# Kernel tuning notes

Hardware: AMD Instinct MI355X
Metric: run time of the kernel (lower is better)

## Reference

```python
import jax, jax.numpy as jnp
import numpy as np

K = 3
EPS = 1e-16

def setup_inputs() -> dict:
    key = jax.random.key(0)
    k1, k2, k3 = jax.random.split(key, 3)
    x = jax.random.normal(k1, (4096, 256), dtype=jnp.float32)
    pos_l = jax.random.normal(k2, (4096, 3), dtype=jnp.float32)
    pos_h = jax.random.normal(k3, (16384, 3), dtype=jnp.float32)
    return {"x": x, "pos_l": pos_l, "pos_h": pos_h}

def reference(x, pos_l, pos_h):
    # Squared pairwise distances [N_h, N_l] via expansion (GEMM-friendly)
    d2 = (jnp.sum(pos_h * pos_h, axis=1)[:, None]
          - 2.0 * pos_h @ pos_l.T
          + jnp.sum(pos_l * pos_l, axis=1)[None, :])
    # k nearest coarse neighbors per fine point
    _, idx = jax.lax.top_k(-d2, K)                      # idx: [N_h, K]
    # Recompute exact squared distances for selected neighbors (matches PyG knn_interpolate)
    diff = pos_h[:, None, :] - pos_l[idx]               # [N_h, K, D]
    d2_sel = jnp.sum(diff * diff, axis=-1)              # [N_h, K]
    w = 1.0 / jnp.clip(d2_sel, EPS)                     # inverse-distance weights
    feats = x[idx]                                      # [N_h, K, F]
    y = jnp.sum(feats * w[:, :, None], axis=1) / jnp.sum(w, axis=1, keepdims=True)
    return y
```

## Files before the change

kernel.cpp:

```cpp
#include <hip/hip_runtime.h>
#include <math.h>

#define NL    4096
#define NH    16384
#define NF4   64
#define BLK   1024
#define NW    16
#define FPB   64
#define PERW  (NL / NW)
#define TOPM  5
#define SENT  0x7fffffff

typedef float v8f __attribute__((ext_vector_type(8)));
typedef float v2f __attribute__((ext_vector_type(2)));

__device__ __forceinline__ int med3i(int a, int b, int c)
{
  int d;
  asm("v_med3_i32 %0, %1, %2, %3" : "=v"(d) : "v"(a), "v"(b), "v"(c));
  return d;
}
__device__ __forceinline__ int mini(int a, int b)
{
  int d;
  asm("v_min_i32 %0, %1, %2" : "=v"(d) : "v"(a), "v"(b));
  return d;
}
__device__ __forceinline__ void ins5(int k, int& b0, int& b1, int& b2,
                                     int& b3, int& b4)
{
  const int n0 = mini(b0, k);
  const int n1 = med3i(k, b0, b1);
  const int n2 = med3i(k, b1, b2);
  const int n3 = med3i(k, b2, b3);
  const int n4 = med3i(k, b3, b4);
  b0 = n0; b1 = n1; b2 = n2; b3 = n3; b4 = n4;
}

__device__ __forceinline__ void lexins3(float d, int j,
    float& b0, float& b1, float& b2, int& i0, int& i1, int& i2)
{
  bool s2 = (d < b2) || ((d == b2) && (j < i2));
  b2 = s2 ? d : b2;  i2 = s2 ? j : i2;
  bool s1 = (b2 < b1) || ((b2 == b1) && (i2 < i1));
  float tf = b1; int ti = i1;
  b1 = s1 ? b2 : b1;  i1 = s1 ? i2 : i1;
  b2 = s1 ? tf : b2;  i2 = s1 ? ti : i2;
  bool s0 = (b1 < b0) || ((b1 == b0) && (i1 < i0));
  tf = b0; ti = i0;
  b0 = s0 ? b1 : b0;  i0 = s0 ? i1 : i0;
  b1 = s0 ? tf : b1;  i1 = s0 ? ti : i1;
}

__device__ __forceinline__ v2f dist2_pk(v2f lx, v2f ly, v2f lz, v2f ll,
                                        v2f h00, v2f h11, v2f h22, v2f hhh,
                                        v2f m22)
{
  v2f d;
  asm("v_pk_mul_f32 %0, %1, %2\n\t"
      "v_pk_fma_f32 %0, %3, %4, %0\n\t"
      "v_pk_fma_f32 %0, %5, %6, %0\n\t"
      "v_pk_fma_f32 %0, %0, %7, %8\n\t"
      "v_pk_add_f32 %0, %0, %9"
      : "=&v"(d)
      : "v"(h00), "s"(lx), "v"(h11), "s"(ly), "v"(h22), "s"(lz),
        "v"(m22), "v"(hhh), "s"(ll));
  return d;
}

#define LOADCH(X, Y, Z, W, P)                                   \
  asm volatile("s_load_dwordx8 %0, %4, 0x0\n\t"                 \
               "s_load_dwordx8 %1, %4, 0x4000\n\t"              \
               "s_load_dwordx8 %2, %4, 0x8000\n\t"              \
               "s_load_dwordx8 %3, %4, 0xc000"                  \
               : "=&s"(X), "=&s"(Y), "=&s"(Z), "=&s"(W)         \
               : "s"(P))
#define WAITCH(X, Y, Z, W)                                      \
  asm volatile("s_waitcnt lgkmcnt(0)"                           \
               : "+s"(X), "+s"(Y), "+s"(Z), "+s"(W))

__global__ __launch_bounds__(256)
void prep_soa_kernel(const float* __restrict__ pos_l, float* __restrict__ cand)
{
  const int i = blockIdx.x * 256 + threadIdx.x;
  const float l0 = pos_l[i * 3 + 0];
  const float l1 = pos_l[i * 3 + 1];
  const float l2 = pos_l[i * 3 + 2];
  const float ll = __fadd_rn(__fadd_rn(__fmul_rn(l0, l0), __fmul_rn(l1, l1)),
                             __fmul_rn(l2, l2));
  cand[i]          = l0;
  cand[NL + i]     = l1;
  cand[2 * NL + i] = l2;
  cand[3 * NL + i] = ll;
}

__global__ __launch_bounds__(BLK)
void knn_interp_kernel(const float* __restrict__ x,
                       const float* __restrict__ pos_l,
                       const float* __restrict__ pos_h,
                       const float* __restrict__ cand,
                       float* __restrict__ out)
{
  __shared__ int   pk_[NW * FPB * TOPM];
  __shared__ float wn[FPB * 3];
  __shared__ int   sj[FPB * 3];

  const int tid  = threadIdx.x;
  const int lane = tid & 63;
  const int wv   = __builtin_amdgcn_readfirstlane(tid >> 6);
  const int fg   = blockIdx.x * FPB + lane;

  const float h0 = pos_h[fg * 3 + 0];
  const float h1 = pos_h[fg * 3 + 1];
  const float h2 = pos_h[fg * 3 + 2];
  const float hh = __fadd_rn(__fadd_rn(__fmul_rn(h0, h0), __fmul_rn(h1, h1)),
                             __fmul_rn(h2, h2));
  const v2f h00 = { h0, h0 }, h11 = { h1, h1 }, h22 = { h2, h2 };
  const v2f hhh = { hh, hh }, m22 = { -2.0f, -2.0f };

  unsigned int kmaskv;
  asm("v_mov_b32 %0, 0xfffff000" : "=v"(kmaskv));

  int a0 = SENT, a1 = SENT, a2 = SENT, a3 = SENT, a4 = SENT;
  int c0 = SENT, c1 = SENT, c2 = SENT, c3 = SENT, c4 = SENT;

  const int jbase = __builtin_amdgcn_readfirstlane(wv * PERW);

#define EVAL8(X, Y, Z, W, JB)                                              \
  do {                                                                     \
    _Pragma("unroll")                                                      \
    for (int pr = 0; pr < 4; ++pr) {                                       \
      const v2f lx = { X[2 * pr], X[2 * pr + 1] };                         \
      const v2f ly = { Y[2 * pr], Y[2 * pr + 1] };                         \
      const v2f lz = { Z[2 * pr], Z[2 * pr + 1] };                         \
      const v2f lw = { W[2 * pr], W[2 * pr + 1] };                         \
      const v2f d  = dist2_pk(lx, ly, lz, lw, h00, h11, h22, hhh, m22);    \
      const int j0 = (JB) + 2 * pr;                                        \
      const int j1 = j0 + 1;                                               \
      int k0, k1;                                                          \
      asm("v_and_or_b32 %0, %1, %2, %3"                                    \
          : "=v"(k0) : "v"(d.x), "v"(kmaskv), "s"(j0));                    \
      asm("v_and_or_b32 %0, %1, %2, %3"                                    \
          : "=v"(k1) : "v"(d.y), "v"(kmaskv), "s"(j1));                    \
      ins5(k0, a0, a1, a2, a3, a4);                                        \
      ins5(k1, c0, c1, c2, c3, c4);                                        \
    }                                                                      \
  } while (0)

  {
    v8f ax_, ay_, az_, aw_, bx_, by_, bz_, bw_;
    LOADCH(ax_, ay_, az_, aw_, cand + jbase);
    for (int t = 0; t < PERW; t += 16) {
      WAITCH(ax_, ay_, az_, aw_);
      LOADCH(bx_, by_, bz_, bw_, cand + jbase + t + 8);
      EVAL8(ax_, ay_, az_, aw_, jbase + t);
      WAITCH(bx_, by_, bz_, bw_);
      LOADCH(ax_, ay_, az_, aw_, cand + jbase + t + 16);
      EVAL8(bx_, by_, bz_, bw_, jbase + t + 8);
    }
  }
#undef EVAL8

  ins5(c0, a0, a1, a2, a3, a4);
  ins5(c1, a0, a1, a2, a3, a4);
  ins5(c2, a0, a1, a2, a3, a4);
  ins5(c3, a0, a1, a2, a3, a4);
  ins5(c4, a0, a1, a2, a3, a4);

  {
    const int s = (wv * FPB + lane) * TOPM;
    pk_[s + 0] = a0; pk_[s + 1] = a1; pk_[s + 2] = a2;
    pk_[s + 3] = a3; pk_[s + 4] = a4;
  }
  __syncthreads();

  if (tid < FPB) {
    int m0 = SENT, m1 = SENT, m2 = SENT, m3 = SENT, m4 = SENT;
    for (int w = 0; w < NW; ++w) {
      const int s = (w * FPB + tid) * TOPM;
      #pragma unroll
      for (int q = 0; q < TOPM; ++q)
        ins5(pk_[s + q], m0, m1, m2, m3, m4);
    }

    float e0 = INFINITY, e1 = INFINITY, e2 = INFINITY;
    int   i0 = 0x7fffffff, i1 = 0x7fffffff, i2 = 0x7fffffff;
    const int mk[TOPM] = { m0, m1, m2, m3, m4 };
    #pragma unroll
    for (int q = 0; q < TOPM; ++q) {
      const int j = mk[q] & 0xFFF;
      const float lx = cand[j];
      const float ly = cand[NL + j];
      const float lz = cand[2 * NL + j];
      const float ll = cand[3 * NL + j];
      const float dot = __fmaf_rn(h2, lz, __fmaf_rn(h1, ly, __fmul_rn(h0, lx)));
      const float d2  = __fadd_rn(__fsub_rn(hh, __fmul_rn(2.0f, dot)), ll);
      lexins3(d2, j, e0, e1, e2, i0, i1, i2);
    }

    const int fm = blockIdx.x * FPB + tid;
    const float H0 = pos_h[fm * 3 + 0];
    const float H1 = pos_h[fm * 3 + 1];
    const float H2 = pos_h[fm * 3 + 2];
    float wk[3];
    int   jk[3] = { i0, i1, i2 };
    #pragma unroll
    for (int k = 0; k < 3; ++k) {
      const int j = jk[k];
      const float dx = __fsub_rn(H0, pos_l[j * 3 + 0]);
      const float dy = __fsub_rn(H1, pos_l[j * 3 + 1]);
      const float dz = __fsub_rn(H2, pos_l[j * 3 + 2]);
      float d2 = __fadd_rn(__fadd_rn(__fmul_rn(dx, dx), __fmul_rn(dy, dy)),
                           __fmul_rn(dz, dz));
      d2 = fmaxf(d2, 1e-16f);
      wk[k] = __frcp_rn(d2);
    }
    const float W  = __fadd_rn(__fadd_rn(wk[0], wk[1]), wk[2]);
    const float rW = __frcp_rn(W);
    #pragma unroll
    for (int k = 0; k < 3; ++k) {
      wn[tid * 3 + k] = wk[k] * rW;
      sj[tid * 3 + k] = jk[k];
    }
  }
  __syncthreads();

  const float4* __restrict__ x4   = (const float4*)x;
  float4* __restrict__       out4 = (float4*)out;
  #pragma unroll
  for (int i = 0; i < (FPB * NF4) / BLK; ++i) {
    const int task = tid + i * BLK;
    const int f    = task >> 6;
    const int cc   = task & 63;
    const int j0 = sj[f * 3 + 0], j1 = sj[f * 3 + 1], j2 = sj[f * 3 + 2];
    const float w0 = wn[f * 3 + 0], w1 = wn[f * 3 + 1], w2 = wn[f * 3 + 2];
    const float4 xa = x4[j0 * NF4 + cc];
    const float4 xb = x4[j1 * NF4 + cc];
    const float4 xc = x4[j2 * NF4 + cc];
    float4 r;
    r.x = xa.x * w0 + xb.x * w1 + xc.x * w2;
    r.y = xa.y * w0 + xb.y * w1 + xc.y * w2;
    r.z = xa.z * w0 + xb.z * w1 + xc.z * w2;
    r.w = xa.w * w0 + xb.w * w1 + xc.w * w2;
    out4[(blockIdx.x * FPB + f) * NF4 + cc] = r;
  }
}

extern "C" void kernel_launch(void* const* d_in, const int* in_sizes, int n_in,
                              void* d_out, int out_size, void* d_ws, size_t ws_size,
                              hipStream_t stream)
{
  const float* x     = (const float*)d_in[0];
  const float* pos_l = (const float*)d_in[1];
  const float* pos_h = (const float*)d_in[2];
  float* out  = (float*)d_out;
  float* cand = (float*)d_ws;

  hipLaunchKernelGGL(prep_soa_kernel, dim3(NL / 256), dim3(256), 0, stream,
                     pos_l, cand);
  hipLaunchKernelGGL(knn_interp_kernel, dim3(NH / FPB), dim3(BLK), 0, stream,
                     x, pos_l, pos_h, cand, out);
}
```

Baseline: 91.98 us.

## Split candidate scan across two blocks per fine group and add finish kernel

Each group of 64 fine points is now handled by two blocks, each scanning half of the coarse points. Each block writes its top-5 keys to a workspace buffer. A separate finish kernel merges the two partial lists, picks the exact top-3, and does the weighted feature gather. This doubles the block count from 256 to 512 so more CUs stay busy on the 256-CU MI355X. The cost is an extra kernel launch, a global round trip for the keys, and recomputing the squared norms from pos_l in the finish kernel.

```diff
diff --git a/kernel.cpp b/kernel.cpp
--- a/kernel.cpp
+++ b/kernel.cpp
@@ -7,7 +7,8 @@
 #define BLK   1024
 #define NW    16
 #define FPB   64
-#define PERW  (NL / NW)
+#define NHALF 2048
+#define SLICE (NHALF / NW)
 #define TOPM  5
 #define SENT  0x7fffffff
 
@@ -95,20 +96,18 @@
 }
 
 __global__ __launch_bounds__(BLK)
-void knn_interp_kernel(const float* __restrict__ x,
-                       const float* __restrict__ pos_l,
-                       const float* __restrict__ pos_h,
-                       const float* __restrict__ cand,
-                       float* __restrict__ out)
-{
-  __shared__ int   pk_[NW * FPB * TOPM];
-  __shared__ float wn[FPB * 3];
-  __shared__ int   sj[FPB * 3];
+void knn_scan_kernel(const float* __restrict__ pos_h,
+                     const float* __restrict__ cand,
+                     int* __restrict__ pkeys)
+{
+  __shared__ int pk_[NW * FPB * TOPM];
 
   const int tid  = threadIdx.x;
   const int lane = tid & 63;
   const int wv   = __builtin_amdgcn_readfirstlane(tid >> 6);
-  const int fg   = blockIdx.x * FPB + lane;
+  const int half = blockIdx.x & 1;
+  const int fgrp = blockIdx.x >> 1;
+  const int fg   = fgrp * FPB + lane;
 
   const float h0 = pos_h[fg * 3 + 0];
   const float h1 = pos_h[fg * 3 + 1];
@@ -124,7 +123,7 @@
   int a0 = SENT, a1 = SENT, a2 = SENT, a3 = SENT, a4 = SENT;
   int c0 = SENT, c1 = SENT, c2 = SENT, c3 = SENT, c4 = SENT;
 
-  const int jbase = __builtin_amdgcn_readfirstlane(wv * PERW);
+  const int jbase = __builtin_amdgcn_readfirstlane(half * NHALF + wv * SLICE);
 
 #define EVAL8(X, Y, Z, W, JB)                                              \
   do {                                                                     \
@@ -150,7 +149,7 @@
   {
     v8f ax_, ay_, az_, aw_, bx_, by_, bz_, bw_;
     LOADCH(ax_, ay_, az_, aw_, cand + jbase);
-    for (int t = 0; t < PERW; t += 16) {
+    for (int t = 0; t < SLICE; t += 16) {
       WAITCH(ax_, ay_, az_, aw_);
       LOADCH(bx_, by_, bz_, bw_, cand + jbase + t + 8);
       EVAL8(ax_, ay_, az_, aw_, jbase + t);
@@ -158,6 +157,7 @@
       LOADCH(ax_, ay_, az_, aw_, cand + jbase + t + 16);
       EVAL8(bx_, by_, bz_, bw_, jbase + t + 8);
     }
+    WAITCH(ax_, ay_, az_, aw_);
   }
 #undef EVAL8
 
@@ -182,34 +182,59 @@
       for (int q = 0; q < TOPM; ++q)
         ins5(pk_[s + q], m0, m1, m2, m3, m4);
     }
+    const int o = (half * NH + fgrp * FPB + tid) * TOPM;
+    pkeys[o + 0] = m0; pkeys[o + 1] = m1; pkeys[o + 2] = m2;
+    pkeys[o + 3] = m3; pkeys[o + 4] = m4;
+  }
+}
+
+__global__ __launch_bounds__(BLK)
+void knn_finish_kernel(const float* __restrict__ x,
+                       const float* __restrict__ pos_l,
+                       const float* __restrict__ pos_h,
+                       const int* __restrict__ pkeys,
+                       float* __restrict__ out)
+{
+  __shared__ float wn[FPB * 3];
+  __shared__ int   sj[FPB * 3];
+  const int tid = threadIdx.x;
+
+  if (tid < FPB) {
+    const int f = blockIdx.x * FPB + tid;
+    const float h0 = pos_h[f * 3 + 0];
+    const float h1 = pos_h[f * 3 + 1];
+    const float h2 = pos_h[f * 3 + 2];
+    const float hh = __fadd_rn(__fadd_rn(__fmul_rn(h0, h0), __fmul_rn(h1, h1)),
+                               __fmul_rn(h2, h2));
 
     float e0 = INFINITY, e1 = INFINITY, e2 = INFINITY;
     int   i0 = 0x7fffffff, i1 = 0x7fffffff, i2 = 0x7fffffff;
-    const int mk[TOPM] = { m0, m1, m2, m3, m4 };
     #pragma unroll
-    for (int q = 0; q < TOPM; ++q) {
-      const int j = mk[q] & 0xFFF;
-      const float lx = cand[j];
-      const float ly = cand[NL + j];
-      const float lz = cand[2 * NL + j];
-      const float ll = cand[3 * NL + j];
-      const float dot = __fmaf_rn(h2, lz, __fmaf_rn(h1, ly, __fmul_rn(h0, lx)));
-      const float d2  = __fadd_rn(__fsub_rn(hh, __fmul_rn(2.0f, dot)), ll);
-      lexins3(d2, j, e0, e1, e2, i0, i1, i2);
-    }
-
-    const int fm = blockIdx.x * FPB + tid;
-    const float H0 = pos_h[fm * 3 + 0];
-    const float H1 = pos_h[fm * 3 + 1];
-    const float H2 = pos_h[fm * 3 + 2];
+    for (int hset = 0; hset < 2; ++hset) {
+      const int o = (hset * NH + f) * TOPM;
+      #pragma unroll
+      for (int q = 0; q < TOPM; ++q) {
+        const int j = pkeys[o + q] & 0xFFF;
+        const float lx = pos_l[j * 3 + 0];
+        const float ly = pos_l[j * 3 + 1];
+        const float lz = pos_l[j * 3 + 2];
+        const float ll = __fadd_rn(__fadd_rn(__fmul_rn(lx, lx),
+                                             __fmul_rn(ly, ly)),
+                                   __fmul_rn(lz, lz));
+        const float dot = __fmaf_rn(h2, lz, __fmaf_rn(h1, ly, __fmul_rn(h0, lx)));
+        const float d2  = __fadd_rn(__fsub_rn(hh, __fmul_rn(2.0f, dot)), ll);
+        lexins3(d2, j, e0, e1, e2, i0, i1, i2);
+      }
+    }
+
     float wk[3];
     int   jk[3] = { i0, i1, i2 };
     #pragma unroll
     for (int k = 0; k < 3; ++k) {
       const int j = jk[k];
-      const float dx = __fsub_rn(H0, pos_l[j * 3 + 0]);
-      const float dy = __fsub_rn(H1, pos_l[j * 3 + 1]);
-      const float dz = __fsub_rn(H2, pos_l[j * 3 + 2]);
+      const float dx = __fsub_rn(h0, pos_l[j * 3 + 0]);
+      const float dy = __fsub_rn(h1, pos_l[j * 3 + 1]);
+      const float dz = __fsub_rn(h2, pos_l[j * 3 + 2]);
       float d2 = __fadd_rn(__fadd_rn(__fmul_rn(dx, dx), __fmul_rn(dy, dy)),
                            __fmul_rn(dz, dz));
       d2 = fmaxf(d2, 1e-16f);
@@ -253,11 +278,14 @@
   const float* x     = (const float*)d_in[0];
   const float* pos_l = (const float*)d_in[1];
   const float* pos_h = (const float*)d_in[2];
-  float* out  = (float*)d_out;
-  float* cand = (float*)d_ws;
+  float* out   = (float*)d_out;
+  float* cand  = (float*)d_ws;
+  int*   pkeys = (int*)(cand + 4 * NL);
 
   hipLaunchKernelGGL(prep_soa_kernel, dim3(NL / 256), dim3(256), 0, stream,
                      pos_l, cand);
-  hipLaunchKernelGGL(knn_interp_kernel, dim3(NH / FPB), dim3(BLK), 0, stream,
-                     x, pos_l, pos_h, cand, out);
-}
+  hipLaunchKernelGGL(knn_scan_kernel, dim3((NH / FPB) * 2), dim3(BLK), 0,
+                     stream, pos_h, cand, pkeys);
+  hipLaunchKernelGGL(knn_finish_kernel, dim3(NH / FPB), dim3(BLK), 0, stream,
+                     x, pos_l, pos_h, pkeys, out);
+}
```

Result: slower. 94.67 us (+2.9%).
